# Performance work log

Hardware: AMD Instinct MI355X
Metric: run time of the kernel (lower is better)

## Reference

```python
import jax, jax.numpy as jnp
import numpy as np

NUM_HEADS = 32
NUM_KV_HEADS = 8
HEAD_DIM = 128
SEQ = 2048
MAX_SLOTS = 4096
SCALE = float(1.0 / np.sqrt(HEAD_DIM))  # attn_scale
G = NUM_HEADS // NUM_KV_HEADS  # num_queries_per_kv


def setup_inputs() -> dict:
    key = jax.random.key(0)
    k1, k2, k3 = jax.random.split(key, 3)
    q = jax.random.normal(k1, (SEQ, NUM_HEADS, HEAD_DIM), dtype=jnp.float32)
    k = jax.random.normal(k2, (SEQ, NUM_KV_HEADS, HEAD_DIM), dtype=jnp.float32)
    v = jax.random.normal(k3, (SEQ, NUM_KV_HEADS, HEAD_DIM), dtype=jnp.float32)
    k_cache = jnp.zeros((MAX_SLOTS, NUM_KV_HEADS, HEAD_DIM), dtype=jnp.float32)
    v_cache = jnp.zeros((MAX_SLOTS, NUM_KV_HEADS, HEAD_DIM), dtype=jnp.float32)
    slot_mapping = jnp.arange(SEQ, dtype=jnp.int64)  # contiguous block_table slots
    return {"q": q, "k": k, "v": v, "k_cache": k_cache, "v_cache": v_cache,
            "slot_mapping": slot_mapping}


def reference(q, k, v, k_cache, v_cache, slot_mapping):
    # prefill: scatter-write new K/V into the paged cache (self.k_cache[slot_mapping] = k)
    kc = k_cache.at[slot_mapping].set(k)
    vc = v_cache.at[slot_mapping].set(v)
    # gather K/V back from the cache via slot mapping (paged gather pattern)
    k_attn = kc[slot_mapping]  # (S, Hkv, D) == k since slots are unique
    v_attn = vc[slot_mapping]
    # GQA: repeat_interleave kv heads to match query heads
    kr = jnp.repeat(k_attn, G, axis=1)  # (S, H, D)
    vr = jnp.repeat(v_attn, G, axis=1)
    # scores: (H, Sq, Sk), naive full materialization as in the original
    scores = jnp.einsum('qhd,khd->hqk', q, kr) * SCALE
    sq, sk = q.shape[0], k_attn.shape[0]
    mask = jnp.tril(jnp.ones((sq, sk), dtype=bool))  # causal (num_query_tokens > 1)
    scores = jnp.where(mask[None, :, :], scores, -jnp.inf)
    weights = jax.nn.softmax(scores, axis=-1)
    out = jnp.einsum('hqk,khd->qhd', weights, vr)  # (S, H, D)
    return out
```

## Files before the change

### kernel.cpp

```cpp
#include <hip/hip_runtime.h>
#include <hip/hip_bf16.h>

#define SEQ 2048
#define QSTR 4096
#define CSCALE 0.1275174364688796f

typedef __attribute__((ext_vector_type(8)))  short short8;
typedef __attribute__((ext_vector_type(4)))  float f32x4;
typedef __attribute__((ext_vector_type(16))) float f32x16;

union PF8 { unsigned u[4]; short8 s; };

__device__ __forceinline__ unsigned short f2bf(float f) {
    union { __hip_bfloat16 b; unsigned short u; } cv;
    cv.b = __float2bfloat16(f);
    return cv.u;
}

__device__ __forceinline__ void gload16(const unsigned short* g, unsigned short* l) {
    __builtin_amdgcn_global_load_lds(
        (const __attribute__((address_space(1))) void*)g,
        (__attribute__((address_space(3))) void*)l, 16, 0, 0);
}

__global__ void prep_k(const float* __restrict__ Kg, unsigned short* __restrict__ Kb) {
    int gi = blockIdx.x * 256 + threadIdx.x;
    int kv = gi >> 8;
    int rem = gi & 255;
    int hk = rem >> 5;
    int d4 = rem & 31;
    f32x4 k4 = *(const f32x4*)(Kg + ((size_t)kv * 8 + hk) * 128 + 4 * d4);
    ushort4 u = make_ushort4(f2bf(k4[0]), f2bf(k4[1]), f2bf(k4[2]), f2bf(k4[3]));
    *(ushort4*)(Kb + ((size_t)hk * SEQ + kv) * 128 + 4 * d4) = u;
}

__global__ void prep_v(const float* __restrict__ Vg, unsigned short* __restrict__ Vtb) {
    const int hk  = blockIdx.x >> 5;
    const int kvb = blockIdx.x & 31;
    __shared__ unsigned short T[128][72];
    const int t = threadIdx.x;
    #pragma unroll
    for (int i = 0; i < 8; ++i) {
        int idx = t + 256 * i;
        int r = idx >> 5, d4 = idx & 31;
        f32x4 v = *(const f32x4*)(Vg + ((size_t)(kvb * 64 + r) * 8 + hk) * 128 + 4 * d4);
        T[4 * d4 + 0][r] = f2bf(v[0]);
        T[4 * d4 + 1][r] = f2bf(v[1]);
        T[4 * d4 + 2][r] = f2bf(v[2]);
        T[4 * d4 + 3][r] = f2bf(v[3]);
    }
    __syncthreads();
    #pragma unroll
    for (int i = 0; i < 8; ++i) {
        int idx = t + 256 * i;
        int d = idx >> 4, c4 = idx & 15;
        ushort4 u = *(ushort4*)&T[d][4 * c4];
        *(ushort4*)(Vtb + ((size_t)hk * 128 + d) * SEQ + kvb * 64 + 4 * c4) = u;
    }
}

__launch_bounds__(256, 2)
__global__ void attn_fwd(const float* __restrict__ Qg,
                         const unsigned short* __restrict__ Kb,
                         const unsigned short* __restrict__ Vtb,
                         float* __restrict__ Og) {
    const int bid = blockIdx.x;
    const int qb  = bid >> 5;
    const int h   = bid & 31;
    const int hk  = h >> 2;
    const int tid  = threadIdx.x;
    const int w    = tid >> 6;
    const int lane = tid & 63;
    const int q5   = lane & 31;
    const int t5   = lane >> 5;
    const int swz  = lane & 7;

    __shared__ __align__(16) unsigned char smem[67584];
    typedef unsigned short KsT[64][128];
    typedef unsigned short VtT[128][64];
    KsT* Ks = (KsT*)smem;
    VtT* Vt = (VtT*)(smem + 32768);
    float (*Ot)[132] = (float(*)[132])smem;

    const int qblk = (w >> 1) ? (31 - qb) : qb;
    const int q0w  = qblk * 64 + 32 * (w & 1);
    const int nt   = 32 - qb;

    short8 qf[8];
    {
        const float* qp = Qg + (size_t)(q0w + q5) * QSTR + h * 128 + 8 * t5;
        #pragma unroll
        for (int st = 0; st < 8; ++st) {
            f32x4 a = *(const f32x4*)(qp + 16 * st);
            f32x4 b = *(const f32x4*)(qp + 16 * st + 4);
            short8 f;
            f[0] = (short)f2bf(a[0] * CSCALE); f[1] = (short)f2bf(a[1] * CSCALE);
            f[2] = (short)f2bf(a[2] * CSCALE); f[3] = (short)f2bf(a[3] * CSCALE);
            f[4] = (short)f2bf(b[0] * CSCALE); f[5] = (short)f2bf(b[1] * CSCALE);
            f[6] = (short)f2bf(b[2] * CSCALE); f[7] = (short)f2bf(b[3] * CSCALE);
            qf[st] = f;
        }
    }
    #pragma unroll
    for (int st = 0; st < 8; ++st) asm volatile("" :: "v"(qf[st]));
    asm volatile("s_waitcnt vmcnt(0)" ::: "memory");

    f32x16 oacc[4];
    #pragma unroll
    for (int dt = 0; dt < 4; ++dt)
        #pragma unroll
        for (int r = 0; r < 16; ++r) oacc[dt][r] = 0.f;
    float m = -1e30f, l = 0.f;

    auto ISSUE = [&](int t, int b) {
        const int kv0 = t * 64;
        #pragma unroll
        for (int p = 0; p < 4; ++p) {
            int row = 16 * w + 4 * p + (lane >> 4);
            const unsigned short* g = Kb +
                ((size_t)hk * SEQ + kv0 + row) * 128 + 8 * ((lane & 15) ^ (row & 7));
            gload16(g, &Ks[b][16 * w + 4 * p][0]);
        }
        #pragma unroll
        for (int p = 0; p < 4; ++p) {
            int d = 32 * w + 8 * p + (lane >> 3);
            const unsigned short* g = Vtb +
                ((size_t)hk * 128 + d) * SEQ + kv0 + 8 * ((lane & 7) ^ (d & 7));
            gload16(g, &Vt[b][32 * w + 8 * p][0]);
        }
    };

    ISSUE(0, 0);
    ISSUE(1, 1);

    for (int t = 0; t < nt; ++t) {
        const int kv0 = t * 64;
        const int buf = t & 1;
        if (t + 1 < nt) asm volatile("s_waitcnt vmcnt(8)" ::: "memory");
        else            asm volatile("s_waitcnt vmcnt(0)" ::: "memory");
        __builtin_amdgcn_s_barrier();

        const bool active = (kv0 <= q0w + 31);
        if (active) {
            f32x16 sac[2];
            __builtin_amdgcn_s_setprio(1);
            #pragma unroll
            for (int kvs = 0; kvs < 2; ++kvs) {
                f32x16 acc;
                #pragma unroll
                for (int r = 0; r < 16; ++r) acc[r] = 0.f;
                #pragma unroll
                for (int st = 0; st < 8; ++st) {
                    short8 kf = *(const short8*)
                        &Ks[buf][32 * kvs + q5][8 * ((2 * st + t5) ^ swz)];
                    acc = __builtin_amdgcn_mfma_f32_32x32x16_bf16(kf, qf[st], acc, 0, 0, 0);
                }
                sac[kvs] = acc;
            }
            __builtin_amdgcn_s_setprio(0);

            if (kv0 + 63 > q0w) {
                const int qrow = q0w + q5;
                #pragma unroll
                for (int kvs = 0; kvs < 2; ++kvs)
                    #pragma unroll
                    for (int r = 0; r < 16; ++r) {
                        int kv = kv0 + 32 * kvs + (r & 3) + 8 * (r >> 2) + 4 * t5;
                        if (kv > qrow) sac[kvs][r] = -1e30f;
                    }
            }

            float t16[16], t8[8], t4[4], t2[2];
            #pragma unroll
            for (int i = 0; i < 16; ++i) t16[i] = fmaxf(sac[0][i], sac[1][i]);
            #pragma unroll
            for (int i = 0; i < 8; ++i) t8[i] = fmaxf(t16[i], t16[i + 8]);
            #pragma unroll
            for (int i = 0; i < 4; ++i) t4[i] = fmaxf(t8[i], t8[i + 4]);
            t2[0] = fmaxf(t4[0], t4[2]); t2[1] = fmaxf(t4[1], t4[3]);
            float mx = fmaxf(t2[0], t2[1]);
            mx = fmaxf(mx, __shfl_xor(mx, 32));

            const bool skip = __all(mx <= m + 11.0f);
            float fac = 1.0f;
            if (!skip) {
                float mn = fmaxf(m, mx);
                fac = exp2f(m - mn);
                m = mn;
            }

            float ps;
            {
                #pragma unroll
                for (int kvs = 0; kvs < 2; ++kvs)
                    #pragma unroll
                    for (int r = 0; r < 16; ++r)
                        sac[kvs][r] = exp2f(sac[kvs][r] - m);
                float s16[16], s8[8], s4[4], s2[2];
                #pragma unroll
                for (int i = 0; i < 16; ++i) s16[i] = sac[0][i] + sac[1][i];
                #pragma unroll
                for (int i = 0; i < 8; ++i) s8[i] = s16[i] + s16[i + 8];
                #pragma unroll
                for (int i = 0; i < 4; ++i) s4[i] = s8[i] + s8[i + 4];
                s2[0] = s4[0] + s4[2]; s2[1] = s4[1] + s4[3];
                ps = s2[0] + s2[1];
                ps += __shfl_xor(ps, 32);
            }
            if (!skip) {
                l = l * fac + ps;
                #pragma unroll
                for (int dt = 0; dt < 4; ++dt)
                    #pragma unroll
                    for (int r = 0; r < 16; ++r) oacc[dt][r] *= fac;
            } else {
                l += ps;
            }

            unsigned pkw[2][8];
            #pragma unroll
            for (int a = 0; a < 2; ++a)
                #pragma unroll
                for (int rp = 0; rp < 8; ++rp)
                    pkw[a][rp] = (unsigned)f2bf(sac[a][2 * rp]) |
                                 ((unsigned)f2bf(sac[a][2 * rp + 1]) << 16);

            unsigned xp[2][8];
            #pragma unroll
            for (int a = 0; a < 2; ++a)
                #pragma unroll
                for (int i = 0; i < 8; ++i)
                    xp[a][i] = (unsigned)__shfl_xor((int)pkw[a][i], 32);

            PF8 pf[4];
            #pragma unroll
            for (int ks = 0; ks < 4; ++ks) {
                const int a = ks >> 1;
                #pragma unroll
                for (int j = 0; j < 4; ++j) {
                    const int ib = (j & 1) + 4 * (ks & 1);
                    const unsigned own_lo = pkw[a][ib];
                    const unsigned own_hi = pkw[a][ib + 2];
                    const unsigned par_lo = xp[a][ib];
                    const unsigned par_hi = xp[a][ib + 2];
                    pf[ks].u[j] = (j < 2) ? (t5 ? par_hi : own_lo)
                                          : (t5 ? own_hi : par_lo);
                }
            }

            __builtin_amdgcn_s_setprio(1);
            #pragma unroll
            for (int dt = 0; dt < 4; ++dt) {
                #pragma unroll
                for (int ks = 0; ks < 4; ++ks) {
                    short8 vf = *(const short8*)
                        &Vt[buf][32 * dt + q5][8 * ((2 * ks + t5) ^ swz)];
                    oacc[dt] = __builtin_amdgcn_mfma_f32_32x32x16_bf16(vf, pf[ks].s, oacc[dt], 0, 0, 0);
                }
            }
            __builtin_amdgcn_s_setprio(0);
        }

        asm volatile("" ::: "memory");
        __builtin_amdgcn_s_barrier();
        if (t + 2 < nt) ISSUE(t + 2, buf);
    }

    asm volatile("" ::: "memory");
    const float rl = 1.0f / l;
    #pragma unroll
    for (int dt = 0; dt < 4; ++dt)
        #pragma unroll
        for (int b = 0; b < 4; ++b) {
            f32x4 v;
            v[0] = oacc[dt][4 * b + 0] * rl;
            v[1] = oacc[dt][4 * b + 1] * rl;
            v[2] = oacc[dt][4 * b + 2] * rl;
            v[3] = oacc[dt][4 * b + 3] * rl;
            *(f32x4*)&Ot[32 * w + q5][32 * dt + 8 * b + 4 * t5] = v;
        }
    __syncthreads();
    {
        const int col4 = (tid & 31) * 4;
        const int r0   = tid >> 5;
        float* ob = Og + h * 128;
        #pragma unroll
        for (int i = 0; i < 16; ++i) {
            int row = 8 * i + r0;
            int grow = (row < 64) ? (qb * 64 + row) : ((31 - qb) * 64 + row - 64);
            f32x4 v = *(const f32x4*)&Ot[row][col4];
            *(f32x4*)(ob + (size_t)grow * QSTR + col4) = v;
        }
    }
}

extern "C" void kernel_launch(void* const* d_in, const int* in_sizes, int n_in,
                              void* d_out, int out_size, void* d_ws, size_t ws_size,
                              hipStream_t stream) {
    const float* q = (const float*)d_in[0];
    const float* k = (const float*)d_in[1];
    const float* v = (const float*)d_in[2];
    float* out = (float*)d_out;
    unsigned short* Kb  = (unsigned short*)d_ws;
    unsigned short* Vtb = Kb + (size_t)8 * SEQ * 128;
    prep_k<<<dim3(2048), 256, 0, stream>>>(k, Kb);
    prep_v<<<dim3(256), 256, 0, stream>>>(v, Vtb);
    attn_fwd<<<dim3(512), 256, 0, stream>>>(q, Kb, Vtb, out);
}
```

Measured before the change: 98.31 us.

## Restructure attention into 512-thread blocks with split-KV waves and paired q-blocks

Each block now uses 512 threads (8 waves) and processes two 128-row query blocks in sequence (a balanced pair), with KV tiles of 128 split across two wave groups that each own half the keys. A split-softmax merge epilogue combines the partial m/l/O of the two KV halves through shared memory. Grid halves to 256 blocks. The aim is larger KV tiles for more reuse per load, and better causal load balance. The cost is about 150KB of LDS, which limits occupancy to one block per CU, plus extra barriers in the merge.

```diff
diff --git a/kernel.cpp b/kernel.cpp
--- a/kernel.cpp
+++ b/kernel.cpp
@@ -59,36 +59,39 @@
     }
 }
 
-__launch_bounds__(256, 2)
+__launch_bounds__(512, 2)
 __global__ void attn_fwd(const float* __restrict__ Qg,
                          const unsigned short* __restrict__ Kb,
                          const unsigned short* __restrict__ Vtb,
                          float* __restrict__ Og) {
     const int bid = blockIdx.x;
-    const int qb  = bid >> 5;
+    const int pr  = bid >> 5;
     const int h   = bid & 31;
     const int hk  = h >> 2;
+    const int QBb = 15 - pr;
+    const int QBa = pr;
+    const int nsB = QBb + 1;
+
     const int tid  = threadIdx.x;
     const int w    = tid >> 6;
+    const int wq   = w & 3;
+    const int wk   = w >> 2;
     const int lane = tid & 63;
     const int q5   = lane & 31;
     const int t5   = lane >> 5;
     const int swz  = lane & 7;
 
-    __shared__ __align__(16) unsigned char smem[67584];
-    typedef unsigned short KsT[64][128];
-    typedef unsigned short VtT[128][64];
-    KsT* Ks = (KsT*)smem;
-    VtT* Vt = (VtT*)(smem + 32768);
-    float (*Ot)[132] = (float(*)[132])smem;
-
-    const int qblk = (w >> 1) ? (31 - qb) : qb;
-    const int q0w  = qblk * 64 + 32 * (w & 1);
-    const int nt   = 32 - qb;
+    __shared__ __align__(16) unsigned char smem[150016];
+    typedef unsigned short TileT[128][128];
+    TileT* Ks = (TileT*)smem;
+    TileT* Vt = (TileT*)(smem + 65536);
+    float* mlm = (float*)(smem + 131072);
+    float* mll = (float*)(smem + 132096);
+    float (*Ot)[132] = (float(*)[132])(smem + 133120);
 
     short8 qf[8];
-    {
-        const float* qp = Qg + (size_t)(q0w + q5) * QSTR + h * 128 + 8 * t5;
+    auto LOADQ = [&](int QB) __attribute__((always_inline)) {
+        const float* qp = Qg + (size_t)(QB * 128 + 32 * wq + q5) * QSTR + h * 128 + 8 * t5;
         #pragma unroll
         for (int st = 0; st < 8; ++st) {
             f32x4 a = *(const f32x4*)(qp + 16 * st);
@@ -100,48 +103,132 @@
             f[6] = (short)f2bf(b[2] * CSCALE); f[7] = (short)f2bf(b[3] * CSCALE);
             qf[st] = f;
         }
-    }
+    };
+
+    auto ISSUE = [&](int kv0, int b) __attribute__((always_inline)) {
+        #pragma unroll
+        for (int p4 = 0; p4 < 4; ++p4) {
+            int row = 16 * w + 4 * p4 + (lane >> 4);
+            const unsigned short* g = Kb +
+                ((size_t)hk * SEQ + kv0 + row) * 128 + 8 * ((lane & 15) ^ (row & 7));
+            gload16(g, &Ks[b][16 * w + 4 * p4][0]);
+        }
+        #pragma unroll
+        for (int p4 = 0; p4 < 4; ++p4) {
+            int d = 16 * w + 4 * p4 + (lane >> 4);
+            const unsigned short* g = Vtb +
+                ((size_t)hk * 128 + d) * SEQ + kv0 + 8 * ((lane & 15) ^ (d & 7));
+            gload16(g, &Vt[b][16 * w + 4 * p4][0]);
+        }
+    };
+
+    f32x16 oacc[4];
+    float m, l;
+    auto RESET = [&]() __attribute__((always_inline)) {
+        #pragma unroll
+        for (int dt = 0; dt < 4; ++dt)
+            #pragma unroll
+            for (int r = 0; r < 16; ++r) oacc[dt][r] = 0.f;
+        m = -1e30f; l = 0.f;
+    };
+
+    auto EPI = [&](int QBp) __attribute__((always_inline)) {
+        if (t5 == 0) mlm[w * 32 + q5] = m;
+        asm volatile("s_waitcnt lgkmcnt(0)" ::: "memory");
+        __builtin_amdgcn_sched_barrier(0);
+        __builtin_amdgcn_s_barrier();
+        const float mOth = mlm[(w ^ 4) * 32 + q5];
+        const float M  = fmaxf(m, mOth);
+        const float sc = exp2f(m - M);
+        const float lp = l * sc;
+        #pragma unroll
+        for (int dt = 0; dt < 4; ++dt)
+            #pragma unroll
+            for (int r = 0; r < 16; ++r) oacc[dt][r] *= sc;
+        if (t5 == 0) mll[w * 32 + q5] = lp;
+        asm volatile("s_waitcnt lgkmcnt(0)" ::: "memory");
+        __builtin_amdgcn_sched_barrier(0);
+        __builtin_amdgcn_s_barrier();
+        const float lOth = mll[(w ^ 4) * 32 + q5];
+
+        #pragma unroll 1
+        for (int tq = 0; tq < 4; ++tq) {
+            if (w == tq + 4) {
+                #pragma unroll
+                for (int dt = 0; dt < 4; ++dt)
+                    #pragma unroll
+                    for (int b = 0; b < 4; ++b) {
+                        f32x4 v;
+                        v[0] = oacc[dt][4 * b + 0]; v[1] = oacc[dt][4 * b + 1];
+                        v[2] = oacc[dt][4 * b + 2]; v[3] = oacc[dt][4 * b + 3];
+                        *(f32x4*)&Ot[q5][32 * dt + 8 * b + 4 * t5] = v;
+                    }
+            }
+            asm volatile("s_waitcnt lgkmcnt(0)" ::: "memory");
+            __builtin_amdgcn_sched_barrier(0);
+            __builtin_amdgcn_s_barrier();
+            if (w == tq) {
+                const float rl = 1.0f / (lp + lOth);
+                #pragma unroll
+                for (int dt = 0; dt < 4; ++dt)
+                    #pragma unroll
+                    for (int b = 0; b < 4; ++b) {
+                        f32x4 o1 = *(const f32x4*)&Ot[q5][32 * dt + 8 * b + 4 * t5];
+                        f32x4 oc;
+                        oc[0] = (oacc[dt][4 * b + 0] + o1[0]) * rl;
+                        oc[1] = (oacc[dt][4 * b + 1] + o1[1]) * rl;
+                        oc[2] = (oacc[dt][4 * b + 2] + o1[2]) * rl;
+                        oc[3] = (oacc[dt][4 * b + 3] + o1[3]) * rl;
+                        *(f32x4*)&Ot[q5][32 * dt + 8 * b + 4 * t5] = oc;
+                    }
+            }
+            asm volatile("s_waitcnt lgkmcnt(0)" ::: "memory");
+            __builtin_amdgcn_sched_barrier(0);
+            __builtin_amdgcn_s_barrier();
+            {
+                float* ob = Og + (size_t)(QBp * 128 + 32 * tq) * QSTR + h * 128;
+                #pragma unroll
+                for (int i = 0; i < 2; ++i) {
+                    int u  = tid + 512 * i;
+                    int r  = u >> 5;
+                    int c4 = (u & 31) * 4;
+                    f32x4 v = *(const f32x4*)&Ot[r][c4];
+                    *(f32x4*)(ob + (size_t)r * QSTR + c4) = v;
+                }
+            }
+            asm volatile("s_waitcnt lgkmcnt(0)" ::: "memory");
+            __builtin_amdgcn_sched_barrier(0);
+            __builtin_amdgcn_s_barrier();
+        }
+    };
+
+    LOADQ(QBb);
     #pragma unroll
     for (int st = 0; st < 8; ++st) asm volatile("" :: "v"(qf[st]));
     asm volatile("s_waitcnt vmcnt(0)" ::: "memory");
-
-    f32x16 oacc[4];
-    #pragma unroll
-    for (int dt = 0; dt < 4; ++dt)
-        #pragma unroll
-        for (int r = 0; r < 16; ++r) oacc[dt][r] = 0.f;
-    float m = -1e30f, l = 0.f;
-
-    auto ISSUE = [&](int t, int b) {
-        const int kv0 = t * 64;
-        #pragma unroll
-        for (int p = 0; p < 4; ++p) {
-            int row = 16 * w + 4 * p + (lane >> 4);
-            const unsigned short* g = Kb +
-                ((size_t)hk * SEQ + kv0 + row) * 128 + 8 * ((lane & 15) ^ (row & 7));
-            gload16(g, &Ks[b][16 * w + 4 * p][0]);
-        }
-        #pragma unroll
-        for (int p = 0; p < 4; ++p) {
-            int d = 32 * w + 8 * p + (lane >> 3);
-            const unsigned short* g = Vtb +
-                ((size_t)hk * 128 + d) * SEQ + kv0 + 8 * ((lane & 7) ^ (d & 7));
-            gload16(g, &Vt[b][32 * w + 8 * p][0]);
-        }
-    };
+    RESET();
 
     ISSUE(0, 0);
-    ISSUE(1, 1);
-
-    for (int t = 0; t < nt; ++t) {
-        const int kv0 = t * 64;
-        const int buf = t & 1;
-        if (t + 1 < nt) asm volatile("s_waitcnt vmcnt(8)" ::: "memory");
+    ISSUE(128, 1);
+
+    for (int s = 0; s < 17; ++s) {
+        if (s == nsB) {
+            LOADQ(QBa);
+            EPI(QBb);
+            RESET();
+        }
+        const bool isB = (s < nsB);
+        const int kv0   = isB ? 128 * s : 128 * (s - nsB);
+        const int q0blk = isB ? 128 * QBb : 128 * QBa;
+        const int buf = s & 1;
+
+        if (s + 1 < 17) asm volatile("s_waitcnt vmcnt(8)" ::: "memory");
         else            asm volatile("s_waitcnt vmcnt(0)" ::: "memory");
         __builtin_amdgcn_s_barrier();
 
-        const bool active = (kv0 <= q0w + 31);
-        if (active) {
+        const int q0w = q0blk + 32 * wq;
+        const int kvb = kv0 + 64 * wk;
+        if (kvb <= q0w + 31) {
             f32x16 sac[2];
             __builtin_amdgcn_s_setprio(1);
             #pragma unroll
@@ -152,20 +239,20 @@
                 #pragma unroll
                 for (int st = 0; st < 8; ++st) {
                     short8 kf = *(const short8*)
-                        &Ks[buf][32 * kvs + q5][8 * ((2 * st + t5) ^ swz)];
+                        &Ks[buf][64 * wk + 32 * kvs + q5][8 * ((2 * st + t5) ^ swz)];
                     acc = __builtin_amdgcn_mfma_f32_32x32x16_bf16(kf, qf[st], acc, 0, 0, 0);
                 }
                 sac[kvs] = acc;
             }
             __builtin_amdgcn_s_setprio(0);
 
-            if (kv0 + 63 > q0w) {
+            if (kvb + 63 > q0w) {
                 const int qrow = q0w + q5;
                 #pragma unroll
                 for (int kvs = 0; kvs < 2; ++kvs)
                     #pragma unroll
                     for (int r = 0; r < 16; ++r) {
-                        int kv = kv0 + 32 * kvs + (r & 3) + 8 * (r >> 2) + 4 * t5;
+                        int kv = kvb + 32 * kvs + (r & 3) + 8 * (r >> 2) + 4 * t5;
                         if (kv > qrow) sac[kvs][r] = -1e30f;
                     }
             }
@@ -254,7 +341,7 @@
                 #pragma unroll
                 for (int ks = 0; ks < 4; ++ks) {
                     short8 vf = *(const short8*)
-                        &Vt[buf][32 * dt + q5][8 * ((2 * ks + t5) ^ swz)];
+                        &Vt[buf][32 * dt + q5][8 * (8 * wk + ((2 * ks + t5) ^ swz))];
                     oacc[dt] = __builtin_amdgcn_mfma_f32_32x32x16_bf16(vf, pf[ks].s, oacc[dt], 0, 0, 0);
                 }
             }
@@ -263,35 +350,13 @@
 
         asm volatile("" ::: "memory");
         __builtin_amdgcn_s_barrier();
-        if (t + 2 < nt) ISSUE(t + 2, buf);
+        if (s + 2 < 17) {
+            const int s2 = s + 2;
+            ISSUE((s2 < nsB) ? 128 * s2 : 128 * (s2 - nsB), s & 1);
+        }
     }
 
-    asm volatile("" ::: "memory");
-    const float rl = 1.0f / l;
-    #pragma unroll
-    for (int dt = 0; dt < 4; ++dt)
-        #pragma unroll
-        for (int b = 0; b < 4; ++b) {
-            f32x4 v;
-            v[0] = oacc[dt][4 * b + 0] * rl;
-            v[1] = oacc[dt][4 * b + 1] * rl;
-            v[2] = oacc[dt][4 * b + 2] * rl;
-            v[3] = oacc[dt][4 * b + 3] * rl;
-            *(f32x4*)&Ot[32 * w + q5][32 * dt + 8 * b + 4 * t5] = v;
-        }
-    __syncthreads();
-    {
-        const int col4 = (tid & 31) * 4;
-        const int r0   = tid >> 5;
-        float* ob = Og + h * 128;
-        #pragma unroll
-        for (int i = 0; i < 16; ++i) {
-            int row = 8 * i + r0;
-            int grow = (row < 64) ? (qb * 64 + row) : ((31 - qb) * 64 + row - 64);
-            f32x4 v = *(const f32x4*)&Ot[row][col4];
-            *(f32x4*)(ob + (size_t)grow * QSTR + col4) = v;
-        }
-    }
+    EPI(QBa);
 }
 
 extern "C" void kernel_launch(void* const* d_in, const int* in_sizes, int n_in,
@@ -305,5 +370,5 @@
     unsigned short* Vtb = Kb + (size_t)8 * SEQ * 128;
     prep_k<<<dim3(2048), 256, 0, stream>>>(k, Kb);
     prep_v<<<dim3(256), 256, 0, stream>>>(v, Vtb);
-    attn_fwd<<<dim3(512), 256, 0, stream>>>(q, Kb, Vtb, out);
-}
+    attn_fwd<<<dim3(256), 512, 0, stream>>>(q, Kb, Vtb, out);
+}
```

Result: faster. 89.29 us (-9.2%).
